# Performance work log

Hardware: AMD Instinct MI355X
Metric: run time of the kernel (lower is better)

The kernel has to match this reference:

```python
import jax, jax.numpy as jnp
import numpy as np

N_NODES = 100000
N_EDGES = 500000
NUM_RADIAL = 6
HIDDEN = 128
VOCAB = 95

def swish(x):
    return x * jax.nn.sigmoid(x)

def setup_inputs() -> dict:
    key = jax.random.key(0)
    ks = jax.random.split(key, 8)
    x = jax.random.randint(ks[0], (N_NODES,), 0, VOCAB)
    rbf = jax.random.normal(ks[1], (N_EDGES, NUM_RADIAL), dtype=jnp.float32)
    i = jax.random.randint(ks[2], (N_EDGES,), 0, N_NODES)
    j = jax.random.randint(ks[3], (N_EDGES,), 0, N_NODES)
    emb_weight = jax.random.uniform(ks[4], (VOCAB, HIDDEN), dtype=jnp.float32,
                                    minval=-np.sqrt(3.0), maxval=np.sqrt(3.0))
    W_rbf = jax.random.normal(ks[5], (HIDDEN, NUM_RADIAL), dtype=jnp.float32) * 0.1
    b_rbf = jnp.zeros((HIDDEN,), dtype=jnp.float32)
    W_lin = jax.random.normal(ks[6], (HIDDEN, 3 * HIDDEN), dtype=jnp.float32) * 0.05
    b_lin = jnp.zeros((HIDDEN,), dtype=jnp.float32)
    return {"x": x, "rbf": rbf, "i": i, "j": j,
            "emb_weight": emb_weight, "W_rbf": W_rbf, "b_rbf": b_rbf,
            "W_lin": W_lin, "b_lin": b_lin}

def reference(x, rbf, i, j, emb_weight, W_rbf, b_rbf, W_lin, b_lin):
    # atom-type embedding lookup: [N, H]
    h = emb_weight[x]
    # rbf projection + swish: [E, H]
    rbf_h = swish(rbf @ W_rbf.T + b_rbf)
    # dual gather + concat: [E, 3H]
    cat = jnp.concatenate([h[i], h[j], rbf_h], axis=-1)
    # linear + swish: [E, H] (dropout in eval mode -> identity)
    out = swish(cat @ W_lin.T + b_lin)
    return out
```

## Files before the change

kernel.cpp:

```cpp
#include <hip/hip_runtime.h>

#define NRAD  6
#define HID   128
#define VOCAB 95
#define EPB   128

__device__ __forceinline__ float swishf(float v) {
    return v * __builtin_amdgcn_rcpf(1.0f + __expf(-v));
}

__global__ void precompute_kernel(const float* __restrict__ emb,
                                  const float* __restrict__ Wl,
                                  const float* __restrict__ bl,
                                  float* __restrict__ A1,
                                  float* __restrict__ A2,
                                  float* __restrict__ W3T)
{
    const int blk = blockIdx.x;
    const int t = threadIdx.x;
    if (blk < VOCAB) {
        __shared__ __align__(16) float se[HID];
        se[t] = emb[blk * HID + t];
        __syncthreads();
        float s1 = bl[t];
        float s2 = 0.0f;
        const float4* w1 = reinterpret_cast<const float4*>(Wl + t * 384);
        const float4* w2 = reinterpret_cast<const float4*>(Wl + t * 384 + 128);
        #pragma unroll
        for (int d4 = 0; d4 < 32; ++d4) {
            float4 a = w1[d4];
            float4 b = w2[d4];
            float e0 = se[d4*4+0], e1 = se[d4*4+1], e2 = se[d4*4+2], e3 = se[d4*4+3];
            s1 += e0*a.x + e1*a.y + e2*a.z + e3*a.w;
            s2 += e0*b.x + e1*b.y + e2*b.z + e3*b.w;
        }
        A1[blk * HID + t] = s1;
        A2[blk * HID + t] = s2;
    } else {
        for (int k = 0; k < HID; ++k)
            W3T[k * HID + t] = Wl[t * 384 + 256 + k];
    }
}

__global__ __launch_bounds__(256, 2) void main_kernel(
    const int*   __restrict__ xidx,
    const float* __restrict__ rbf,
    const int*   __restrict__ ei,
    const int*   __restrict__ ej,
    const float* __restrict__ Wr,
    const float* __restrict__ br,
    const float* __restrict__ A1,
    const float* __restrict__ A2,
    const float* __restrict__ W3T,
    float*       __restrict__ out,
    int E)
{
    __shared__ __align__(16) float sh_h[HID][EPB];
    __shared__ float sh_wr[HID * 7];

    const int tid = threadIdx.x;
    const long eb = (long)blockIdx.x * EPB;

    if (tid < HID) {
        #pragma unroll
        for (int r = 0; r < NRAD; ++r) sh_wr[tid * 7 + r] = Wr[tid * NRAD + r];
        sh_wr[tid * 7 + 6] = br[tid];
    }

    {
        const int el = tid & (EPB - 1);
        const int kg = tid >> 7;
        const long e = eb + el;
        float r0 = 0, r1 = 0, r2 = 0, r3 = 0, r4 = 0, r5 = 0;
        if (e < E) {
            const float* rp = rbf + e * NRAD;
            r0 = rp[0]; r1 = rp[1]; r2 = rp[2]; r3 = rp[3]; r4 = rp[4]; r5 = rp[5];
        }
        __syncthreads();
        #pragma unroll 4
        for (int kk = 0; kk < 64; ++kk) {
            const int k = kg * 64 + kk;
            const float* w = &sh_wr[k * 7];
            float m = w[6] + r0*w[0] + r1*w[1] + r2*w[2] + r3*w[3] + r4*w[4] + r5*w[5];
            sh_h[k][el] = swishf(m);
        }
    }
    __syncthreads();

    const int tc = tid & 15;
    const int te = tid >> 4;
    const int c0 = tc * 8;
    const int e0 = te * 8;

    float acc[8][8];
    #pragma unroll
    for (int a = 0; a < 8; ++a)
        #pragma unroll
        for (int b = 0; b < 8; ++b) acc[a][b] = 0.0f;

    float4 nb0 = *reinterpret_cast<const float4*>(W3T + c0);
    float4 nb1 = *reinterpret_cast<const float4*>(W3T + c0 + 4);

    #pragma unroll 4
    for (int k = 0; k < HID; ++k) {
        float4 b0 = nb0, b1 = nb1;
        if (k + 1 < HID) {
            nb0 = *reinterpret_cast<const float4*>(W3T + (k + 1) * HID + c0);
            nb1 = *reinterpret_cast<const float4*>(W3T + (k + 1) * HID + c0 + 4);
        }
        float4 a0 = *reinterpret_cast<const float4*>(&sh_h[k][e0]);
        float4 a1 = *reinterpret_cast<const float4*>(&sh_h[k][e0 + 4]);
        float av[8] = {a0.x, a0.y, a0.z, a0.w, a1.x, a1.y, a1.z, a1.w};
        float bv[8] = {b0.x, b0.y, b0.z, b0.w, b1.x, b1.y, b1.z, b1.w};
        #pragma unroll
        for (int a = 0; a < 8; ++a)
            #pragma unroll
            for (int b = 0; b < 8; ++b)
                acc[a][b] += av[a] * bv[b];
    }

    #pragma unroll
    for (int le = 0; le < 8; ++le) {
        const long e = eb + e0 + le;
        if (e < E) {
            const int xi = xidx[ei[e]];
            const int xj = xidx[ej[e]];
            const float4* p1 = reinterpret_cast<const float4*>(A1 + xi * HID + c0);
            const float4* p2 = reinterpret_cast<const float4*>(A2 + xj * HID + c0);
            float4 q1a = p1[0], q1b = p1[1];
            float4 q2a = p2[0], q2b = p2[1];
            float4 o0, o1;
            o0.x = swishf(acc[le][0] + q1a.x + q2a.x);
            o0.y = swishf(acc[le][1] + q1a.y + q2a.y);
            o0.z = swishf(acc[le][2] + q1a.z + q2a.z);
            o0.w = swishf(acc[le][3] + q1a.w + q2a.w);
            o1.x = swishf(acc[le][4] + q1b.x + q2b.x);
            o1.y = swishf(acc[le][5] + q1b.y + q2b.y);
            o1.z = swishf(acc[le][6] + q1b.z + q2b.z);
            o1.w = swishf(acc[le][7] + q1b.w + q2b.w);
            *reinterpret_cast<float4*>(out + e * HID + c0)     = o0;
            *reinterpret_cast<float4*>(out + e * HID + c0 + 4) = o1;
        }
    }
}

extern "C" void kernel_launch(void* const* d_in, const int* in_sizes, int n_in,
                              void* d_out, int out_size, void* d_ws, size_t ws_size,
                              hipStream_t stream) {
    const int*   x   = (const int*)  d_in[0];
    const float* rbf = (const float*)d_in[1];
    const int*   ei  = (const int*)  d_in[2];
    const int*   ej  = (const int*)  d_in[3];
    const float* emb = (const float*)d_in[4];
    const float* Wr  = (const float*)d_in[5];
    const float* br  = (const float*)d_in[6];
    const float* Wl  = (const float*)d_in[7];
    const float* bl  = (const float*)d_in[8];
    float* out = (float*)d_out;

    const int E = in_sizes[1] / NRAD;

    float* A1  = (float*)d_ws;
    float* A2  = A1 + VOCAB * HID;
    float* W3T = A2 + VOCAB * HID;

    precompute_kernel<<<VOCAB + 1, HID, 0, stream>>>(emb, Wl, bl, A1, A2, W3T);

    const int nblk = (E + EPB - 1) / EPB;
    main_kernel<<<nblk, 256, 0, stream>>>(x, rbf, ei, ej, Wr, br, A1, A2, W3T, out, E);
}
```

Before: 499.1 us.

## Use bf16 MFMA for rbf-hidden GEMM with register-built A fragments

Replaces the scalar FP32 outer-product GEMM over the rbf-projected hidden features with bf16 MFMA 16x16x32 instructions. W3 is pre-converted to bf16 in the precompute kernel, and each wave computes its swish(rbf projection) values directly into MFMA A-fragment registers rather than staging a 64KB shared tile. The epilogue writes per-lane scalar outputs instead of float4. The aim is to cut FP32 FMA work and shared-memory traffic, at the cost of bf16 precision in the GEMM and less vectorized output stores.

```diff
diff --git a/kernel.cpp b/kernel.cpp
--- a/kernel.cpp
+++ b/kernel.cpp
@@ -1,12 +1,23 @@
 #include <hip/hip_runtime.h>
+#include <hip/hip_bf16.h>
 
 #define NRAD  6
 #define HID   128
 #define VOCAB 95
 #define EPB   128
 
+typedef __attribute__((ext_vector_type(4))) float f32x4;
+typedef __attribute__((ext_vector_type(8))) short short8;
+
 __device__ __forceinline__ float swishf(float v) {
     return v * __builtin_amdgcn_rcpf(1.0f + __expf(-v));
+}
+
+__device__ __forceinline__ unsigned short bfbits(float x) {
+    __hip_bfloat16 b = __float2bfloat16(x);
+    unsigned short u;
+    __builtin_memcpy(&u, &b, 2);
+    return u;
 }
 
 __global__ void precompute_kernel(const float* __restrict__ emb,
@@ -14,7 +25,7 @@
                                   const float* __restrict__ bl,
                                   float* __restrict__ A1,
                                   float* __restrict__ A2,
-                                  float* __restrict__ W3T)
+                                  unsigned short* __restrict__ W3bf)
 {
     const int blk = blockIdx.x;
     const int t = threadIdx.x;
@@ -37,8 +48,14 @@
         A1[blk * HID + t] = s1;
         A2[blk * HID + t] = s2;
     } else {
-        for (int k = 0; k < HID; ++k)
-            W3T[k * HID + t] = Wl[t * 384 + 256 + k];
+        #pragma unroll 4
+        for (int k4 = 0; k4 < 32; ++k4) {
+            const float4 v = *reinterpret_cast<const float4*>(Wl + t * 384 + 256 + k4 * 4);
+            uint2 pr;
+            pr.x = (unsigned)bfbits(v.x) | ((unsigned)bfbits(v.y) << 16);
+            pr.y = (unsigned)bfbits(v.z) | ((unsigned)bfbits(v.w) << 16);
+            *reinterpret_cast<uint2*>(W3bf + t * HID + k4 * 4) = pr;
+        }
     }
 }
 
@@ -51,95 +68,116 @@
     const float* __restrict__ br,
     const float* __restrict__ A1,
     const float* __restrict__ A2,
-    const float* __restrict__ W3T,
+    const unsigned short* __restrict__ W3bf,
     float*       __restrict__ out,
     int E)
 {
-    __shared__ __align__(16) float sh_h[HID][EPB];
-    __shared__ float sh_wr[HID * 7];
-
-    const int tid = threadIdx.x;
-    const long eb = (long)blockIdx.x * EPB;
-
-    if (tid < HID) {
-        #pragma unroll
-        for (int r = 0; r < NRAD; ++r) sh_wr[tid * 7 + r] = Wr[tid * NRAD + r];
-        sh_wr[tid * 7 + 6] = br[tid];
-    }
-
-    {
-        const int el = tid & (EPB - 1);
-        const int kg = tid >> 7;
-        const long e = eb + el;
-        float r0 = 0, r1 = 0, r2 = 0, r3 = 0, r4 = 0, r5 = 0;
-        if (e < E) {
-            const float* rp = rbf + e * NRAD;
-            r0 = rp[0]; r1 = rp[1]; r2 = rp[2]; r3 = rp[3]; r4 = rp[4]; r5 = rp[5];
-        }
-        __syncthreads();
-        #pragma unroll 4
-        for (int kk = 0; kk < 64; ++kk) {
-            const int k = kg * 64 + kk;
-            const float* w = &sh_wr[k * 7];
-            float m = w[6] + r0*w[0] + r1*w[1] + r2*w[2] + r3*w[3] + r4*w[4] + r5*w[5];
-            sh_h[k][el] = swishf(m);
-        }
-    }
+    __shared__ __align__(16) float sh_rbf[EPB * 8];
+    __shared__ __align__(16) float sh_wr[HID * 8];
+
+    const int tid  = threadIdx.x;
+    const int lane = tid & 63;
+    const int wid  = tid >> 6;
+    const int wrh  = wid >> 1;
+    const int wch  = wid & 1;
+    const int g    = lane >> 4;
+    const int lm   = lane & 15;
+
+    const long base = (long)blockIdx.x * EPB;
+
+    short8 bfr[4][4];
+    #pragma unroll
+    for (int nf = 0; nf < 4; ++nf)
+        #pragma unroll
+        for (int kf = 0; kf < 4; ++kf) {
+            const int c = wch * 64 + nf * 16 + lm;
+            const int k = kf * 32 + g * 8;
+            bfr[nf][kf] = *reinterpret_cast<const short8*>(W3bf + c * HID + k);
+        }
+
+    #pragma unroll
+    for (int it = 0; it < 3; ++it) {
+        const int idx = tid + it * 256;
+        const long gi = base * NRAD + idx;
+        const float v = (gi < (long)E * NRAD) ? rbf[gi] : 0.0f;
+        sh_rbf[(idx / NRAD) * 8 + idx % NRAD] = v;
+    }
+    #pragma unroll
+    for (int it = 0; it < 3; ++it) {
+        const int idx = tid + it * 256;
+        sh_wr[(idx / NRAD) * 8 + idx % NRAD] = Wr[idx];
+    }
+    if (tid < HID) sh_wr[tid * 8 + 6] = br[tid];
     __syncthreads();
 
-    const int tc = tid & 15;
-    const int te = tid >> 4;
-    const int c0 = tc * 8;
-    const int e0 = te * 8;
-
-    float acc[8][8];
-    #pragma unroll
-    for (int a = 0; a < 8; ++a)
-        #pragma unroll
-        for (int b = 0; b < 8; ++b) acc[a][b] = 0.0f;
-
-    float4 nb0 = *reinterpret_cast<const float4*>(W3T + c0);
-    float4 nb1 = *reinterpret_cast<const float4*>(W3T + c0 + 4);
-
-    #pragma unroll 4
-    for (int k = 0; k < HID; ++k) {
-        float4 b0 = nb0, b1 = nb1;
-        if (k + 1 < HID) {
-            nb0 = *reinterpret_cast<const float4*>(W3T + (k + 1) * HID + c0);
-            nb1 = *reinterpret_cast<const float4*>(W3T + (k + 1) * HID + c0 + 4);
-        }
-        float4 a0 = *reinterpret_cast<const float4*>(&sh_h[k][e0]);
-        float4 a1 = *reinterpret_cast<const float4*>(&sh_h[k][e0 + 4]);
-        float av[8] = {a0.x, a0.y, a0.z, a0.w, a1.x, a1.y, a1.z, a1.w};
-        float bv[8] = {b0.x, b0.y, b0.z, b0.w, b1.x, b1.y, b1.z, b1.w};
-        #pragma unroll
-        for (int a = 0; a < 8; ++a)
+    float rb[4][6];
+    #pragma unroll
+    for (int m = 0; m < 4; ++m) {
+        const int el = wrh * 64 + m * 16 + lm;
+        const float4 a = *reinterpret_cast<const float4*>(&sh_rbf[el * 8]);
+        const float2 b = *reinterpret_cast<const float2*>(&sh_rbf[el * 8 + 4]);
+        rb[m][0] = a.x; rb[m][1] = a.y; rb[m][2] = a.z;
+        rb[m][3] = a.w; rb[m][4] = b.x; rb[m][5] = b.y;
+    }
+
+    f32x4 acc[4][4];
+    #pragma unroll
+    for (int m = 0; m < 4; ++m)
+        #pragma unroll
+        for (int nf = 0; nf < 4; ++nf)
+            acc[m][nf] = (f32x4){0.f, 0.f, 0.f, 0.f};
+
+    #pragma unroll
+    for (int kf = 0; kf < 4; ++kf) {
+        union { short8 v; unsigned u[4]; } afr[4];
+        #pragma unroll
+        for (int j2 = 0; j2 < 4; ++j2) {
+            const int k0 = kf * 32 + g * 8 + j2 * 2;
+            const float4 wa0 = *reinterpret_cast<const float4*>(&sh_wr[k0 * 8]);
+            const float4 wb0 = *reinterpret_cast<const float4*>(&sh_wr[k0 * 8 + 4]);
+            const float4 wa1 = *reinterpret_cast<const float4*>(&sh_wr[k0 * 8 + 8]);
+            const float4 wb1 = *reinterpret_cast<const float4*>(&sh_wr[k0 * 8 + 12]);
             #pragma unroll
-            for (int b = 0; b < 8; ++b)
-                acc[a][b] += av[a] * bv[b];
-    }
-
-    #pragma unroll
-    for (int le = 0; le < 8; ++le) {
-        const long e = eb + e0 + le;
-        if (e < E) {
-            const int xi = xidx[ei[e]];
-            const int xj = xidx[ej[e]];
-            const float4* p1 = reinterpret_cast<const float4*>(A1 + xi * HID + c0);
-            const float4* p2 = reinterpret_cast<const float4*>(A2 + xj * HID + c0);
-            float4 q1a = p1[0], q1b = p1[1];
-            float4 q2a = p2[0], q2b = p2[1];
-            float4 o0, o1;
-            o0.x = swishf(acc[le][0] + q1a.x + q2a.x);
-            o0.y = swishf(acc[le][1] + q1a.y + q2a.y);
-            o0.z = swishf(acc[le][2] + q1a.z + q2a.z);
-            o0.w = swishf(acc[le][3] + q1a.w + q2a.w);
-            o1.x = swishf(acc[le][4] + q1b.x + q2b.x);
-            o1.y = swishf(acc[le][5] + q1b.y + q2b.y);
-            o1.z = swishf(acc[le][6] + q1b.z + q2b.z);
-            o1.w = swishf(acc[le][7] + q1b.w + q2b.w);
-            *reinterpret_cast<float4*>(out + e * HID + c0)     = o0;
-            *reinterpret_cast<float4*>(out + e * HID + c0 + 4) = o1;
+            for (int m = 0; m < 4; ++m) {
+                float s0 = wb0.z;
+                s0 = fmaf(rb[m][0], wa0.x, s0); s0 = fmaf(rb[m][1], wa0.y, s0);
+                s0 = fmaf(rb[m][2], wa0.z, s0); s0 = fmaf(rb[m][3], wa0.w, s0);
+                s0 = fmaf(rb[m][4], wb0.x, s0); s0 = fmaf(rb[m][5], wb0.y, s0);
+                float s1 = wb1.z;
+                s1 = fmaf(rb[m][0], wa1.x, s1); s1 = fmaf(rb[m][1], wa1.y, s1);
+                s1 = fmaf(rb[m][2], wa1.z, s1); s1 = fmaf(rb[m][3], wa1.w, s1);
+                s1 = fmaf(rb[m][4], wb1.x, s1); s1 = fmaf(rb[m][5], wb1.y, s1);
+                const float p0 = swishf(s0);
+                const float p1 = swishf(s1);
+                afr[m].u[j2] = (unsigned)bfbits(p0) | ((unsigned)bfbits(p1) << 16);
+            }
+        }
+        #pragma unroll
+        for (int m = 0; m < 4; ++m)
+            #pragma unroll
+            for (int nf = 0; nf < 4; ++nf)
+                acc[m][nf] = __builtin_amdgcn_mfma_f32_16x16x32_bf16(
+                                 afr[m].v, bfr[nf][kf], acc[m][nf], 0, 0, 0);
+    }
+
+    #pragma unroll
+    for (int m = 0; m < 4; ++m) {
+        #pragma unroll
+        for (int r = 0; r < 4; ++r) {
+            const int el = wrh * 64 + m * 16 + g * 4 + r;
+            const long e = base + el;
+            if (e < E) {
+                const int xi = xidx[ei[e]];
+                const int xj = xidx[ej[e]];
+                const float* p1 = A1 + xi * HID;
+                const float* p2 = A2 + xj * HID;
+                #pragma unroll
+                for (int nf = 0; nf < 4; ++nf) {
+                    const int c = wch * 64 + nf * 16 + lm;
+                    const float v = acc[m][nf][r] + p1[c] + p2[c];
+                    out[e * HID + c] = swishf(v);
+                }
+            }
         }
     }
 }
@@ -160,12 +198,12 @@
 
     const int E = in_sizes[1] / NRAD;
 
-    float* A1  = (float*)d_ws;
-    float* A2  = A1 + VOCAB * HID;
-    float* W3T = A2 + VOCAB * HID;
-
-    precompute_kernel<<<VOCAB + 1, HID, 0, stream>>>(emb, Wl, bl, A1, A2, W3T);
+    float* A1 = (float*)d_ws;
+    float* A2 = A1 + VOCAB * HID;
+    unsigned short* W3bf = (unsigned short*)(A2 + VOCAB * HID);
+
+    precompute_kernel<<<VOCAB + 1, HID, 0, stream>>>(emb, Wl, bl, A1, A2, W3bf);
 
     const int nblk = (E + EPB - 1) / EPB;
-    main_kernel<<<nblk, 256, 0, stream>>>(x, rbf, ei, ej, Wr, br, A1, A2, W3T, out, E);
-}
+    main_kernel<<<nblk, 256, 0, stream>>>(x, rbf, ei, ej, Wr, br, A1, A2, W3bf, out, E);
+}
```

Result: faster. 408.3 us (-18.2%).
